# Performance work log

Measured on AMD Instinct MI355X. Metric: run time of the kernel, lower is better.

Reference implementation:

```python
import jax, jax.numpy as jnp
import numpy as np

D_MODEL = 1024
NUM_HEADS = 16
HEAD_DIM = D_MODEL // NUM_HEADS


def setup_inputs() -> dict:
    key = jax.random.key(0)
    ks = jax.random.split(key, 5)
    x = jax.random.normal(ks[0], (2, 2048, D_MODEL), dtype=jnp.float32)
    # torch nn.Linear init scale ~ U(-1/sqrt(in), 1/sqrt(in)); use small normals
    s = 1.0 / np.sqrt(D_MODEL)
    W_qkv = jax.random.normal(ks[1], (D_MODEL, 3 * D_MODEL), dtype=jnp.float32) * s
    b_qkv = jax.random.normal(ks[2], (3 * D_MODEL,), dtype=jnp.float32) * s
    W_out = jax.random.normal(ks[3], (D_MODEL, D_MODEL), dtype=jnp.float32) * s
    b_out = jax.random.normal(ks[4], (D_MODEL,), dtype=jnp.float32) * s
    return {"x": x, "W_qkv": W_qkv, "b_qkv": b_qkv, "W_out": W_out, "b_out": b_out}


def reference(x, W_qkv, b_qkv, W_out, b_out):
    B, S, _ = x.shape
    qkv = x @ W_qkv + b_qkv                                  # [B,S,3D]
    qkv = qkv.reshape(B, S, NUM_HEADS, 3 * HEAD_DIM).transpose(0, 2, 1, 3)  # [B,H,S,3d]
    q, k, v = jnp.split(qkv, 3, axis=-1)                     # each [B,H,S,d]
    scale = 1.0 / np.sqrt(HEAD_DIM)
    scores = jnp.einsum("bhqd,bhkd->bhqk", q, k) * scale      # [B,H,S,S]
    attn = jax.nn.softmax(scores, axis=-1)
    values = jnp.einsum("bhqk,bhkd->bhqd", attn, v)           # [B,H,S,d]
    values = values.transpose(0, 2, 1, 3).reshape(B, S, D_MODEL)
    return values @ W_out + b_out
```

## Files before the change

### kernel.cpp

```cpp
#include <hip/hip_runtime.h>


#define D_MODEL 1024
#define NHEAD   16
#define HDIM    64
#define SEQ     2048
#define BATCH   2
#define NTOK    (BATCH * SEQ)

typedef float    f32x4 __attribute__((ext_vector_type(4)));
typedef _Float16 f16x8 __attribute__((ext_vector_type(8)));
typedef _Float16 f16x4 __attribute__((ext_vector_type(4)));

#define GLOBAL_LOAD_LDS16(gptr, lptr)                                            \
    __builtin_amdgcn_global_load_lds(                                            \
        (const __attribute__((address_space(1))) unsigned int*)(gptr),           \
        (__attribute__((address_space(3))) unsigned int*)(lptr), 16, 0, 0)

__global__ __launch_bounds__(256) void prep_kernel(
    const float* __restrict__ x, _Float16* __restrict__ xh,
    const float* __restrict__ Wqkv, _Float16* __restrict__ wq_t,
    const float* __restrict__ Wout, _Float16* __restrict__ wo_t)
{
    const int bx = blockIdx.x;
    const int tid = threadIdx.x;
    if (bx < 4096) {
        const int i = (bx * 256 + tid) * 4;
        const float4 v = *(const float4*)&x[i];
        f16x4 hh;
        hh[0] = (_Float16)v.x; hh[1] = (_Float16)v.y;
        hh[2] = (_Float16)v.z; hh[3] = (_Float16)v.w;
        *(f16x4*)&xh[i] = hh;
        return;
    }
    __shared__ float ts[64][65];
    const float* W; _Float16* Wt; int N, n0, k0;
    if (bx < 4096 + 768) {
        const int local = bx - 4096;
        W = Wqkv; Wt = wq_t; N = 3072;
        n0 = (local % 48) * 64; k0 = (local / 48) * 64;
    } else {
        const int local = bx - 4864;
        W = Wout; Wt = wo_t; N = 1024;
        n0 = (local % 16) * 64; k0 = (local / 16) * 64;
    }
    {
        const int r = tid >> 2, c = (tid & 3) << 4;
        const float* src = W + (size_t)(k0 + r) * N + n0 + c;
        #pragma unroll
        for (int u = 0; u < 4; ++u)
            *(float4*)&ts[r][c + u * 4] = *(const float4*)&src[u * 4];
    }
    __syncthreads();
    {
        const int n = tid >> 2, kg = (tid & 3) << 4;
        f16x8 v0, v1;
        #pragma unroll
        for (int j = 0; j < 8; ++j) {
            v0[j] = (_Float16)ts[kg + j][n];
            v1[j] = (_Float16)ts[kg + 8 + j][n];
        }
        _Float16* dst = Wt + (size_t)(n0 + n) * D_MODEL + k0 + kg;
        *(f16x8*)&dst[0] = v0;
        *(f16x8*)&dst[8] = v1;
    }
}

__global__ __launch_bounds__(512) void gemm_qkv_kernel(
    const _Float16* __restrict__ A, const _Float16* __restrict__ Bt,
    const float* __restrict__ bias, _Float16* __restrict__ Cout,
    int M, int N, int K)
{
    __shared__ _Float16 lds[2][4096];
    const int tid = threadIdx.x;
    const int wave = tid >> 6, lane = tid & 63;
    const int quad = lane >> 4, l16 = lane & 15;
    const int m0 = blockIdx.y * 128, n0 = blockIdx.x * 128;
    const int wr = wave >> 1, wc = wave & 1;

    f32x4 acc[2][4] = {};

    const bool isA = wave < 4;
    const _Float16* gsrc = isA ? (A + (size_t)m0 * K) : (Bt + (size_t)n0 * K);
    _Float16* ldst = isA ? &lds[0][0] : &lds[1][0];
    const int sbase = (wave & 3) * 2;

    for (int k0 = 0; k0 < K; k0 += 32) {
        __syncthreads();
        #pragma unroll
        for (int j = 0; j < 2; ++j) {
            const int seg = sbase + j;
            const int chunk = seg >> 1;
            const int row = ((seg & 1) << 6) | lane;
            GLOBAL_LOAD_LDS16(gsrc + (size_t)row * K + k0 + chunk * 8, ldst + seg * 512);
        }
        __syncthreads();

        f16x8 a[2], b[4];
        #pragma unroll
        for (int mt = 0; mt < 2; ++mt)
            a[mt] = *(const f16x8*)&lds[0][quad * 1024 + (wr * 32 + mt * 16 + l16) * 8];
        #pragma unroll
        for (int nt = 0; nt < 4; ++nt)
            b[nt] = *(const f16x8*)&lds[1][quad * 1024 + (wc * 64 + nt * 16 + l16) * 8];
        #pragma unroll
        for (int mt = 0; mt < 2; ++mt)
            #pragma unroll
            for (int nt = 0; nt < 4; ++nt)
                acc[mt][nt] = __builtin_amdgcn_mfma_f32_16x16x32_f16(a[mt], b[nt], acc[mt][nt], 0, 0, 0);
    }

    #pragma unroll
    for (int nt = 0; nt < 4; ++nt) {
        const int col = n0 + wc * 64 + nt * 16 + l16;
        const float bv = bias[col];
        #pragma unroll
        for (int mt = 0; mt < 2; ++mt) {
            #pragma unroll
            for (int r = 0; r < 4; ++r) {
                const int row = m0 + wr * 32 + mt * 16 + quad * 4 + r;
                Cout[(size_t)row * N + col] = (_Float16)(acc[mt][nt][r] + bv);
            }
        }
    }
}

__global__ __launch_bounds__(512) void gemm_out_kernel(
    const _Float16* __restrict__ A, const _Float16* __restrict__ Bt,
    const float* __restrict__ bias, float* __restrict__ Cout)
{
    const int K = D_MODEL, N = D_MODEL;
    __shared__ _Float16 ldsA[4096];
    __shared__ _Float16 ldsB[2048];
    const int tid = threadIdx.x;
    const int wave = tid >> 6, lane = tid & 63;
    const int quad = lane >> 4, l16 = lane & 15;
    const int m0 = blockIdx.y * 128, n0 = blockIdx.x * 64;
    const int wr = wave >> 1, wc = wave & 1;

    f32x4 acc[2][2] = {};

    for (int k0 = 0; k0 < K; k0 += 32) {
        __syncthreads();
        if (wave < 4) {
            #pragma unroll
            for (int j = 0; j < 2; ++j) {
                const int seg = wave * 2 + j;
                const int chunk = seg >> 1;
                const int row = ((seg & 1) << 6) | lane;
                GLOBAL_LOAD_LDS16(A + (size_t)(m0 + row) * K + k0 + chunk * 8, ldsA + seg * 512);
            }
        } else {
            const int seg = wave - 4;
            GLOBAL_LOAD_LDS16(Bt + (size_t)(n0 + lane) * K + k0 + seg * 8, ldsB + seg * 512);
        }
        __syncthreads();

        f16x8 a[2], b[2];
        #pragma unroll
        for (int mt = 0; mt < 2; ++mt)
            a[mt] = *(const f16x8*)&ldsA[quad * 1024 + (wr * 32 + mt * 16 + l16) * 8];
        #pragma unroll
        for (int nt = 0; nt < 2; ++nt)
            b[nt] = *(const f16x8*)&ldsB[quad * 512 + (wc * 32 + nt * 16 + l16) * 8];
        #pragma unroll
        for (int mt = 0; mt < 2; ++mt)
            #pragma unroll
            for (int nt = 0; nt < 2; ++nt)
                acc[mt][nt] = __builtin_amdgcn_mfma_f32_16x16x32_f16(a[mt], b[nt], acc[mt][nt], 0, 0, 0);
    }

    #pragma unroll
    for (int nt = 0; nt < 2; ++nt) {
        const int col = n0 + wc * 32 + nt * 16 + l16;
        const float bv = bias[col];
        #pragma unroll
        for (int mt = 0; mt < 2; ++mt) {
            #pragma unroll
            for (int r = 0; r < 4; ++r) {
                const int row = m0 + wr * 32 + mt * 16 + quad * 4 + r;
                Cout[(size_t)row * N + col] = acc[mt][nt][r] + bv;
            }
        }
    }
}

__global__ __launch_bounds__(256) void swizzle_kv_kernel(
    const _Float16* __restrict__ qkv,
    _Float16* __restrict__ Ksw, _Float16* __restrict__ Vsw)
{
    __shared__ _Float16 ts[64][72];
    const int tid = threadIdx.x;
    const int s0 = blockIdx.x * 64, h = blockIdx.y, b = blockIdx.z;
    const size_t hsz = (size_t)8 * SEQ * 8;
    _Float16* kh = Ksw + (size_t)(b * NHEAD + h) * hsz;
    _Float16* vh = Vsw + (size_t)(b * NHEAD + h) * hsz;

    {
        const int s = s0 + (tid >> 2);
        const int dg = (tid & 3) << 4;
        const _Float16* src = qkv + (size_t)(b * SEQ + s) * (3 * D_MODEL) + h * (3 * HDIM) + HDIM + dg;
        const f16x8 v0 = *(const f16x8*)&src[0];
        const f16x8 v1 = *(const f16x8*)&src[8];
        const int c0 = dg >> 3;
        *(f16x8*)&kh[((size_t)c0 * SEQ + s) * 8]       = v0;
        *(f16x8*)&kh[((size_t)(c0 + 1) * SEQ + s) * 8] = v1;
    }
    {
        const int s = tid >> 2, dg = (tid & 3) << 4;
        const _Float16* src = qkv + (size_t)(b * SEQ + s0 + s) * (3 * D_MODEL) + h * (3 * HDIM) + 2 * HDIM + dg;
        *(f16x8*)&ts[s][dg]     = *(const f16x8*)&src[0];
        *(f16x8*)&ts[s][dg + 8] = *(const f16x8*)&src[8];
    }
    __syncthreads();
    {
        const int d = tid >> 2, sg = (tid & 3) << 4;
        f16x8 v0, v1;
        #pragma unroll
        for (int j = 0; j < 8; ++j) { v0[j] = ts[sg + j][d]; v1[j] = ts[sg + 8 + j][d]; }
        const int cs0 = (s0 + sg) >> 3;
        *(f16x8*)&vh[((size_t)cs0 * HDIM + d) * 8]       = v0;
        *(f16x8*)&vh[((size_t)(cs0 + 1) * HDIM + d) * 8] = v1;
    }
}

__global__ __launch_bounds__(256) void attn_mfma_kernel(
    const _Float16* __restrict__ qkv,
    const _Float16* __restrict__ Ksw, const _Float16* __restrict__ Vsw,
    _Float16* __restrict__ val)
{
    __shared__ _Float16 Ks[8 * 64 * 8];
    __shared__ _Float16 Vts[8 * 64 * 8];
    __shared__ _Float16 Ps[64 * 72];

    const int tid = threadIdx.x;
    const int wave = tid >> 6, lane = tid & 63;
    const int quad = lane >> 4, l16 = lane & 15;
    const int qt = blockIdx.x, h = blockIdx.y, b = blockIdx.z;
    const int q0 = qt * 64;

    const size_t hsz = (size_t)8 * SEQ * 8;
    const _Float16* kh = Ksw + (size_t)(b * NHEAD + h) * hsz;
    const _Float16* vh = Vsw + (size_t)(b * NHEAD + h) * hsz;

    f16x8 qf[2];
    {
        const int row = q0 + wave * 16 + l16;
        const _Float16* src = qkv + (size_t)(b * SEQ + row) * (3 * D_MODEL) + h * (3 * HDIM) + quad * 8;
        const f16x8 t0 = *(const f16x8*)(src);
        const f16x8 t1 = *(const f16x8*)(src + 32);
        #pragma unroll
        for (int j = 0; j < 8; ++j) {
            qf[0][j] = (_Float16)((float)t0[j] * 0.1803368802f);
            qf[1][j] = (_Float16)((float)t1[j] * 0.1803368802f);
        }
    }

    f32x4 acc[4] = {};
    float rs = 0.f;

    for (int kt = 0; kt < SEQ / 64; ++kt) {
        __syncthreads();
        #pragma unroll
        for (int jj = 0; jj < 2; ++jj) {
            const int c = wave * 2 + jj;
            GLOBAL_LOAD_LDS16(kh + ((size_t)c * SEQ + kt * 64 + lane) * 8, Ks + c * 512);
            GLOBAL_LOAD_LDS16(vh + ((size_t)(kt * 8 + c) * HDIM + lane) * 8, Vts + c * 512);
        }
        __syncthreads();

        f32x4 s[4] = {};
        #pragma unroll
        for (int mt = 0; mt < 4; ++mt) {
            const f16x8 kA0 = *(const f16x8*)&Ks[quad * 512 + (mt * 16 + l16) * 8];
            const f16x8 kA1 = *(const f16x8*)&Ks[(4 + quad) * 512 + (mt * 16 + l16) * 8];
            s[mt] = __builtin_amdgcn_mfma_f32_16x16x32_f16(kA0, qf[0], s[mt], 0, 0, 0);
            s[mt] = __builtin_amdgcn_mfma_f32_16x16x32_f16(kA1, qf[1], s[mt], 0, 0, 0);
        }

        #pragma unroll
        for (int mt = 0; mt < 4; ++mt) {
            const float p0 = __builtin_amdgcn_exp2f(s[mt][0]);
            const float p1 = __builtin_amdgcn_exp2f(s[mt][1]);
            const float p2 = __builtin_amdgcn_exp2f(s[mt][2]);
            const float p3 = __builtin_amdgcn_exp2f(s[mt][3]);
            rs += (p0 + p1) + (p2 + p3);
            uint2 w;
            w.x = __builtin_bit_cast(unsigned, __builtin_amdgcn_cvt_pkrtz(p0, p1));
            w.y = __builtin_bit_cast(unsigned, __builtin_amdgcn_cvt_pkrtz(p2, p3));
            *(uint2*)&Ps[(wave * 16 + l16) * 72 + mt * 16 + quad * 4] = w;
        }

        const f16x8 pA0 = *(const f16x8*)&Ps[(wave * 16 + l16) * 72 + quad * 8];
        const f16x8 pA1 = *(const f16x8*)&Ps[(wave * 16 + l16) * 72 + 32 + quad * 8];
        #pragma unroll
        for (int nt = 0; nt < 4; ++nt) {
            const f16x8 v0 = *(const f16x8*)&Vts[quad * 512 + (nt * 16 + l16) * 8];
            const f16x8 v1 = *(const f16x8*)&Vts[(4 + quad) * 512 + (nt * 16 + l16) * 8];
            acc[nt] = __builtin_amdgcn_mfma_f32_16x16x32_f16(pA0, v0, acc[nt], 0, 0, 0);
            acc[nt] = __builtin_amdgcn_mfma_f32_16x16x32_f16(pA1, v1, acc[nt], 0, 0, 0);
        }
    }

    rs += __shfl_xor(rs, 16);
    rs += __shfl_xor(rs, 32);
    const float inv = 1.f / rs;
    float invr[4];
    #pragma unroll
    for (int r = 0; r < 4; ++r)
        invr[r] = __shfl(inv, quad * 4 + r, 16);

    #pragma unroll
    for (int r = 0; r < 4; ++r) {
        const int row = b * SEQ + q0 + wave * 16 + quad * 4 + r;
        #pragma unroll
        for (int nt = 0; nt < 4; ++nt) {
            const int col = h * HDIM + nt * 16 + l16;
            val[(size_t)row * D_MODEL + col] = (_Float16)(acc[nt][r] * invr[r]);
        }
    }
}

extern "C" void kernel_launch(void* const* d_in, const int* in_sizes, int n_in,
                              void* d_out, int out_size, void* d_ws, size_t ws_size,
                              hipStream_t stream)
{
    const float* x     = (const float*)d_in[0];
    const float* W_qkv = (const float*)d_in[1];
    const float* b_qkv = (const float*)d_in[2];
    const float* W_out = (const float*)d_in[3];
    const float* b_out = (const float*)d_in[4];

    char* ws = (char*)d_ws;
    _Float16* Ksw   = (_Float16*)ws;
    _Float16* val_h = (_Float16*)(ws + (8u << 20));
    _Float16* wq_t  = (_Float16*)(ws + (16u << 20));
    _Float16* wo_t  = (_Float16*)(ws + (22u << 20));
    _Float16* qkv_h = (_Float16*)(ws + (24u << 20));
    _Float16* x_h   = (_Float16*)(ws + (48u << 20));
    _Float16* Vsw   = (_Float16*)(ws + (48u << 20));

    prep_kernel<<<5120, 256, 0, stream>>>(x, x_h, W_qkv, wq_t, W_out, wo_t);
    gemm_qkv_kernel<<<dim3(3 * D_MODEL / 128, NTOK / 128), 512, 0, stream>>>(
        x_h, wq_t, b_qkv, qkv_h, NTOK, 3 * D_MODEL, D_MODEL);
    swizzle_kv_kernel<<<dim3(SEQ / 64, NHEAD, BATCH), 256, 0, stream>>>(qkv_h, Ksw, Vsw);
    attn_mfma_kernel<<<dim3(SEQ / 64, NHEAD, BATCH), 256, 0, stream>>>(qkv_h, Ksw, Vsw, val_h);
    gemm_out_kernel<<<dim3(D_MODEL / 64, NTOK / 128), 512, 0, stream>>>(
        val_h, wo_t, b_out, (float*)d_out);
}
```

Baseline: 226.8 us.

## Split KV across waves in attention with cross-wave reduction and MFMA row sums

```diff
diff --git a/kernel.cpp b/kernel.cpp
--- a/kernel.cpp
+++ b/kernel.cpp
@@ -229,94 +229,141 @@
     const _Float16* __restrict__ Ksw, const _Float16* __restrict__ Vsw,
     _Float16* __restrict__ val)
 {
-    __shared__ _Float16 Ks[8 * 64 * 8];
-    __shared__ _Float16 Vts[8 * 64 * 8];
-    __shared__ _Float16 Ps[64 * 72];
+    __shared__ _Float16 Kst[8 * 128 * 8];
+    __shared__ _Float16 Vst[16 * 64 * 8];
+    __shared__ _Float16 Ps[4 * 64 * 40];
 
     const int tid = threadIdx.x;
     const int wave = tid >> 6, lane = tid & 63;
     const int quad = lane >> 4, l16 = lane & 15;
     const int qt = blockIdx.x, h = blockIdx.y, b = blockIdx.z;
     const int q0 = qt * 64;
+    const int wbase = wave * 32;
 
     const size_t hsz = (size_t)8 * SEQ * 8;
     const _Float16* kh = Ksw + (size_t)(b * NHEAD + h) * hsz;
     const _Float16* vh = Vsw + (size_t)(b * NHEAD + h) * hsz;
 
-    f16x8 qf[2];
-    {
-        const int row = q0 + wave * 16 + l16;
+    f16x8 qf[4][2];
+    #pragma unroll
+    for (int nt = 0; nt < 4; ++nt) {
+        const int row = q0 + nt * 16 + l16;
         const _Float16* src = qkv + (size_t)(b * SEQ + row) * (3 * D_MODEL) + h * (3 * HDIM) + quad * 8;
         const f16x8 t0 = *(const f16x8*)(src);
         const f16x8 t1 = *(const f16x8*)(src + 32);
         #pragma unroll
         for (int j = 0; j < 8; ++j) {
-            qf[0][j] = (_Float16)((float)t0[j] * 0.1803368802f);
-            qf[1][j] = (_Float16)((float)t1[j] * 0.1803368802f);
-        }
-    }
-
-    f32x4 acc[4] = {};
-    float rs = 0.f;
-
-    for (int kt = 0; kt < SEQ / 64; ++kt) {
-        __syncthreads();
-        #pragma unroll
-        for (int jj = 0; jj < 2; ++jj) {
-            const int c = wave * 2 + jj;
-            GLOBAL_LOAD_LDS16(kh + ((size_t)c * SEQ + kt * 64 + lane) * 8, Ks + c * 512);
-            GLOBAL_LOAD_LDS16(vh + ((size_t)(kt * 8 + c) * HDIM + lane) * 8, Vts + c * 512);
-        }
-        __syncthreads();
-
-        f32x4 s[4] = {};
-        #pragma unroll
-        for (int mt = 0; mt < 4; ++mt) {
-            const f16x8 kA0 = *(const f16x8*)&Ks[quad * 512 + (mt * 16 + l16) * 8];
-            const f16x8 kA1 = *(const f16x8*)&Ks[(4 + quad) * 512 + (mt * 16 + l16) * 8];
-            s[mt] = __builtin_amdgcn_mfma_f32_16x16x32_f16(kA0, qf[0], s[mt], 0, 0, 0);
-            s[mt] = __builtin_amdgcn_mfma_f32_16x16x32_f16(kA1, qf[1], s[mt], 0, 0, 0);
-        }
-
-        #pragma unroll
-        for (int mt = 0; mt < 4; ++mt) {
-            const float p0 = __builtin_amdgcn_exp2f(s[mt][0]);
-            const float p1 = __builtin_amdgcn_exp2f(s[mt][1]);
-            const float p2 = __builtin_amdgcn_exp2f(s[mt][2]);
-            const float p3 = __builtin_amdgcn_exp2f(s[mt][3]);
-            rs += (p0 + p1) + (p2 + p3);
-            uint2 w;
-            w.x = __builtin_bit_cast(unsigned, __builtin_amdgcn_cvt_pkrtz(p0, p1));
-            w.y = __builtin_bit_cast(unsigned, __builtin_amdgcn_cvt_pkrtz(p2, p3));
-            *(uint2*)&Ps[(wave * 16 + l16) * 72 + mt * 16 + quad * 4] = w;
-        }
-
-        const f16x8 pA0 = *(const f16x8*)&Ps[(wave * 16 + l16) * 72 + quad * 8];
-        const f16x8 pA1 = *(const f16x8*)&Ps[(wave * 16 + l16) * 72 + 32 + quad * 8];
-        #pragma unroll
-        for (int nt = 0; nt < 4; ++nt) {
-            const f16x8 v0 = *(const f16x8*)&Vts[quad * 512 + (nt * 16 + l16) * 8];
-            const f16x8 v1 = *(const f16x8*)&Vts[(4 + quad) * 512 + (nt * 16 + l16) * 8];
-            acc[nt] = __builtin_amdgcn_mfma_f32_16x16x32_f16(pA0, v0, acc[nt], 0, 0, 0);
-            acc[nt] = __builtin_amdgcn_mfma_f32_16x16x32_f16(pA1, v1, acc[nt], 0, 0, 0);
-        }
-    }
-
-    rs += __shfl_xor(rs, 16);
-    rs += __shfl_xor(rs, 32);
-    const float inv = 1.f / rs;
-    float invr[4];
+            qf[nt][0][j] = (_Float16)((float)t0[j] * 0.1803368802f);
+            qf[nt][1][j] = (_Float16)((float)t1[j] * 0.1803368802f);
+        }
+    }
+
+    f16x8 ones;
     #pragma unroll
-    for (int r = 0; r < 4; ++r)
-        invr[r] = __shfl(inv, quad * 4 + r, 16);
-
-    #pragma unroll
-    for (int r = 0; r < 4; ++r) {
-        const int row = b * SEQ + q0 + wave * 16 + quad * 4 + r;
-        #pragma unroll
-        for (int nt = 0; nt < 4; ++nt) {
-            const int col = h * HDIM + nt * 16 + l16;
-            val[(size_t)row * D_MODEL + col] = (_Float16)(acc[nt][r] * invr[r]);
+    for (int j = 0; j < 8; ++j) ones[j] = (_Float16)1.0f;
+
+    f32x4 acc[4][4] = {};
+    f32x4 lones[4] = {};
+
+    _Float16* psw = Ps + wave * (64 * 40);
+
+    for (int kt = 0; kt < SEQ / 128; ++kt) {
+        __syncthreads();
+        #pragma unroll
+        for (int j = 0; j < 4; ++j) {
+            const int kseg = wave * 4 + j;
+            const int c = kseg >> 1, half = kseg & 1;
+            GLOBAL_LOAD_LDS16(kh + ((size_t)c * SEQ + kt * 128 + half * 64 + lane) * 8,
+                              Kst + ((c * 128) + half * 64 + lane) * 8);
+            const int vs = wave * 4 + j;
+            GLOBAL_LOAD_LDS16(vh + ((size_t)(kt * 16 + vs) * 64 + lane) * 8,
+                              Vst + (vs * 64 + lane) * 8);
+        }
+        __syncthreads();
+
+        #pragma unroll
+        for (int mt = 0; mt < 2; ++mt) {
+            const int krow = wbase + mt * 16 + l16;
+            const f16x8 kA0 = *(const f16x8*)&Kst[((quad * 128) + krow) * 8];
+            const f16x8 kA1 = *(const f16x8*)&Kst[(((4 + quad) * 128) + krow) * 8];
+            f32x4 s[4] = {};
+            #pragma unroll
+            for (int nt = 0; nt < 4; ++nt) {
+                s[nt] = __builtin_amdgcn_mfma_f32_16x16x32_f16(kA0, qf[nt][0], s[nt], 0, 0, 0);
+                s[nt] = __builtin_amdgcn_mfma_f32_16x16x32_f16(kA1, qf[nt][1], s[nt], 0, 0, 0);
+            }
+            #pragma unroll
+            for (int nt = 0; nt < 4; ++nt) {
+                const float p0 = __builtin_amdgcn_exp2f(s[nt][0]);
+                const float p1 = __builtin_amdgcn_exp2f(s[nt][1]);
+                const float p2 = __builtin_amdgcn_exp2f(s[nt][2]);
+                const float p3 = __builtin_amdgcn_exp2f(s[nt][3]);
+                uint2 w;
+                w.x = __builtin_bit_cast(unsigned, __builtin_amdgcn_cvt_pkrtz(p0, p1));
+                w.y = __builtin_bit_cast(unsigned, __builtin_amdgcn_cvt_pkrtz(p2, p3));
+                *(uint2*)&psw[(nt * 16 + l16) * 40 + mt * 16 + quad * 4] = w;
+            }
+        }
+
+        f16x8 vf[4];
+        #pragma unroll
+        for (int nt = 0; nt < 4; ++nt)
+            vf[nt] = *(const f16x8*)&Vst[(((wave * 4 + quad) * 64) + nt * 16 + l16) * 8];
+        #pragma unroll
+        for (int mtile = 0; mtile < 4; ++mtile) {
+            const f16x8 pA = *(const f16x8*)&psw[(mtile * 16 + l16) * 40 + quad * 8];
+            #pragma unroll
+            for (int nt = 0; nt < 4; ++nt)
+                acc[mtile][nt] = __builtin_amdgcn_mfma_f32_16x16x32_f16(pA, vf[nt], acc[mtile][nt], 0, 0, 0);
+            lones[mtile] = __builtin_amdgcn_mfma_f32_16x16x32_f16(pA, ones, lones[mtile], 0, 0, 0);
+        }
+    }
+
+    __syncthreads();
+    float* sO = (float*)((wave & 1) ? Vst : Kst);
+    float* sL = ((float*)Ps) + ((wave & 1) ? 64 : 0);
+    if (wave < 2) {
+        #pragma unroll
+        for (int mtile = 0; mtile < 4; ++mtile) {
+            #pragma unroll
+            for (int r = 0; r < 4; ++r) {
+                const int row = mtile * 16 + quad * 4 + r;
+                #pragma unroll
+                for (int nt = 0; nt < 4; ++nt)
+                    sO[row * 64 + nt * 16 + l16] = acc[mtile][nt][r];
+                sL[row] = lones[mtile][r];
+            }
+        }
+    }
+    __syncthreads();
+    if (wave >= 2) {
+        #pragma unroll
+        for (int mtile = 0; mtile < 4; ++mtile) {
+            #pragma unroll
+            for (int r = 0; r < 4; ++r) {
+                const int row = mtile * 16 + quad * 4 + r;
+                #pragma unroll
+                for (int nt = 0; nt < 4; ++nt)
+                    sO[row * 64 + nt * 16 + l16] += acc[mtile][nt][r];
+                sL[row] += lones[mtile][r];
+            }
+        }
+    }
+    __syncthreads();
+    {
+        float* A0 = (float*)Kst; float* A1 = (float*)Vst;
+        float* L = (float*)Ps;
+        #pragma unroll
+        for (int r = 0; r < 4; ++r) {
+            const int row = wave * 16 + quad * 4 + r;
+            const float lt = L[row] + L[64 + row];
+            const float inv = 1.f / lt;
+            _Float16* dst = val + (size_t)(b * SEQ + q0 + row) * D_MODEL + h * HDIM;
+            #pragma unroll
+            for (int c = 0; c < 4; ++c) {
+                const int col = c * 16 + l16;
+                dst[col] = (_Float16)((A0[row * 64 + col] + A1[row * 64 + col]) * inv);
+            }
         }
     }
 }
```

New measurement: 249.0 us. +9.8%, slower.

## Split attention key tiles across waves and reduce partial outputs in LDS

Applied to the files above, without the earlier changes.

```diff
diff --git a/kernel.cpp b/kernel.cpp
--- a/kernel.cpp
+++ b/kernel.cpp
@@ -224,14 +224,15 @@
     }
 }
 
-__global__ __launch_bounds__(256) void attn_mfma_kernel(
+__global__ __launch_bounds__(256, 4) void attn_mfma_kernel(
     const _Float16* __restrict__ qkv,
     const _Float16* __restrict__ Ksw, const _Float16* __restrict__ Vsw,
     _Float16* __restrict__ val)
 {
-    __shared__ _Float16 Ks[8 * 64 * 8];
-    __shared__ _Float16 Vts[8 * 64 * 8];
-    __shared__ _Float16 Ps[64 * 72];
+    __shared__ _Float16 smem[13312];
+    _Float16* Kst = smem;
+    _Float16* Vst = smem + 4096;
+    _Float16* Ps  = smem + 8192;
 
     const int tid = threadIdx.x;
     const int wave = tid >> 6, lane = tid & 63;
@@ -243,81 +244,112 @@
     const _Float16* kh = Ksw + (size_t)(b * NHEAD + h) * hsz;
     const _Float16* vh = Vsw + (size_t)(b * NHEAD + h) * hsz;
 
-    f16x8 qf[2];
-    {
-        const int row = q0 + wave * 16 + l16;
+    f16x8 qf[4][2];
+    #pragma unroll
+    for (int nt = 0; nt < 4; ++nt) {
+        const int row = q0 + nt * 16 + l16;
         const _Float16* src = qkv + (size_t)(b * SEQ + row) * (3 * D_MODEL) + h * (3 * HDIM) + quad * 8;
         const f16x8 t0 = *(const f16x8*)(src);
         const f16x8 t1 = *(const f16x8*)(src + 32);
         #pragma unroll
         for (int j = 0; j < 8; ++j) {
-            qf[0][j] = (_Float16)((float)t0[j] * 0.1803368802f);
-            qf[1][j] = (_Float16)((float)t1[j] * 0.1803368802f);
-        }
-    }
-
-    f32x4 acc[4] = {};
-    float rs = 0.f;
+            qf[nt][0][j] = (_Float16)((float)t0[j] * 0.1803368802f);
+            qf[nt][1][j] = (_Float16)((float)t1[j] * 0.1803368802f);
+        }
+    }
+
+    f32x4 acc[4][4] = {};
+    float rs[4] = {};
+
+    _Float16* psw = Ps + wave * (64 * 20);
 
     for (int kt = 0; kt < SEQ / 64; ++kt) {
         __syncthreads();
         #pragma unroll
-        for (int jj = 0; jj < 2; ++jj) {
-            const int c = wave * 2 + jj;
-            GLOBAL_LOAD_LDS16(kh + ((size_t)c * SEQ + kt * 64 + lane) * 8, Ks + c * 512);
-            GLOBAL_LOAD_LDS16(vh + ((size_t)(kt * 8 + c) * HDIM + lane) * 8, Vts + c * 512);
-        }
-        __syncthreads();
-
-        f32x4 s[4] = {};
-        #pragma unroll
-        for (int mt = 0; mt < 4; ++mt) {
-            const f16x8 kA0 = *(const f16x8*)&Ks[quad * 512 + (mt * 16 + l16) * 8];
-            const f16x8 kA1 = *(const f16x8*)&Ks[(4 + quad) * 512 + (mt * 16 + l16) * 8];
-            s[mt] = __builtin_amdgcn_mfma_f32_16x16x32_f16(kA0, qf[0], s[mt], 0, 0, 0);
-            s[mt] = __builtin_amdgcn_mfma_f32_16x16x32_f16(kA1, qf[1], s[mt], 0, 0, 0);
-        }
-
-        #pragma unroll
-        for (int mt = 0; mt < 4; ++mt) {
-            const float p0 = __builtin_amdgcn_exp2f(s[mt][0]);
-            const float p1 = __builtin_amdgcn_exp2f(s[mt][1]);
-            const float p2 = __builtin_amdgcn_exp2f(s[mt][2]);
-            const float p3 = __builtin_amdgcn_exp2f(s[mt][3]);
-            rs += (p0 + p1) + (p2 + p3);
+        for (int j = 0; j < 2; ++j) {
+            const int c = wave * 2 + j;
+            GLOBAL_LOAD_LDS16(kh + ((size_t)c * SEQ + kt * 64 + lane) * 8, Kst + (c * 64 + lane) * 8);
+            GLOBAL_LOAD_LDS16(vh + ((size_t)(kt * 8 + c) * 64 + lane) * 8, Vst + (c * 64 + lane) * 8);
+        }
+        __syncthreads();
+
+        const f16x8 kA0 = *(const f16x8*)&Kst[(quad * 64 + wave * 16 + l16) * 8];
+        const f16x8 kA1 = *(const f16x8*)&Kst[((4 + quad) * 64 + wave * 16 + l16) * 8];
+        #pragma unroll
+        for (int nt = 0; nt < 4; ++nt) {
+            f32x4 s = {};
+            s = __builtin_amdgcn_mfma_f32_16x16x32_f16(kA0, qf[nt][0], s, 0, 0, 0);
+            s = __builtin_amdgcn_mfma_f32_16x16x32_f16(kA1, qf[nt][1], s, 0, 0, 0);
+            const float p0 = __builtin_amdgcn_exp2f(s[0]);
+            const float p1 = __builtin_amdgcn_exp2f(s[1]);
+            const float p2 = __builtin_amdgcn_exp2f(s[2]);
+            const float p3 = __builtin_amdgcn_exp2f(s[3]);
+            rs[nt] += (p0 + p1) + (p2 + p3);
             uint2 w;
             w.x = __builtin_bit_cast(unsigned, __builtin_amdgcn_cvt_pkrtz(p0, p1));
             w.y = __builtin_bit_cast(unsigned, __builtin_amdgcn_cvt_pkrtz(p2, p3));
-            *(uint2*)&Ps[(wave * 16 + l16) * 72 + mt * 16 + quad * 4] = w;
-        }
-
-        const f16x8 pA0 = *(const f16x8*)&Ps[(wave * 16 + l16) * 72 + quad * 8];
-        const f16x8 pA1 = *(const f16x8*)&Ps[(wave * 16 + l16) * 72 + 32 + quad * 8];
-        #pragma unroll
-        for (int nt = 0; nt < 4; ++nt) {
-            const f16x8 v0 = *(const f16x8*)&Vts[quad * 512 + (nt * 16 + l16) * 8];
-            const f16x8 v1 = *(const f16x8*)&Vts[(4 + quad) * 512 + (nt * 16 + l16) * 8];
-            acc[nt] = __builtin_amdgcn_mfma_f32_16x16x32_f16(pA0, v0, acc[nt], 0, 0, 0);
-            acc[nt] = __builtin_amdgcn_mfma_f32_16x16x32_f16(pA1, v1, acc[nt], 0, 0, 0);
-        }
-    }
-
-    rs += __shfl_xor(rs, 16);
-    rs += __shfl_xor(rs, 32);
-    const float inv = 1.f / rs;
-    float invr[4];
-    #pragma unroll
-    for (int r = 0; r < 4; ++r)
-        invr[r] = __shfl(inv, quad * 4 + r, 16);
-
-    #pragma unroll
-    for (int r = 0; r < 4; ++r) {
-        const int row = b * SEQ + q0 + wave * 16 + quad * 4 + r;
-        #pragma unroll
-        for (int nt = 0; nt < 4; ++nt) {
-            const int col = h * HDIM + nt * 16 + l16;
-            val[(size_t)row * D_MODEL + col] = (_Float16)(acc[nt][r] * invr[r]);
-        }
+            *(uint2*)&psw[(nt * 16 + l16) * 20 + quad * 4] = w;
+        }
+
+        f16x4 vf[4];
+        #pragma unroll
+        for (int nt = 0; nt < 4; ++nt)
+            vf[nt] = *(const f16x4*)&Vst[((wave * 2 + (quad >> 1)) * 64 + nt * 16 + l16) * 8 + (quad & 1) * 4];
+        #pragma unroll
+        for (int mtile = 0; mtile < 4; ++mtile) {
+            const f16x4 pA = *(const f16x4*)&psw[(mtile * 16 + l16) * 20 + quad * 4];
+            #pragma unroll
+            for (int nt = 0; nt < 4; ++nt)
+                acc[mtile][nt] = __builtin_amdgcn_mfma_f32_16x16x16f16(pA, vf[nt], acc[mtile][nt], 0, 0, 0);
+        }
+    }
+
+    __syncthreads();
+    float* sO = (float*)smem;
+    float* sL = (float*)(smem + 8192);
+
+    #pragma unroll
+    for (int nt = 0; nt < 4; ++nt) {
+        rs[nt] += __shfl_xor(rs[nt], 16);
+        rs[nt] += __shfl_xor(rs[nt], 32);
+    }
+    if (quad == 0) {
+        #pragma unroll
+        for (int nt = 0; nt < 4; ++nt)
+            sL[wave * 64 + nt * 16 + l16] = rs[nt];
+    }
+    #pragma unroll
+    for (int w = 0; w < 4; ++w) {
+        if (wave == w) {
+            #pragma unroll
+            for (int mtile = 0; mtile < 4; ++mtile)
+                #pragma unroll
+                for (int r = 0; r < 4; ++r) {
+                    const int row = mtile * 16 + quad * 4 + r;
+                    #pragma unroll
+                    for (int nt = 0; nt < 4; ++nt) {
+                        const int idx = row * 64 + nt * 16 + l16;
+                        if (w == 0) sO[idx] = acc[mtile][nt][r];
+                        else        sO[idx] += acc[mtile][nt][r];
+                    }
+                }
+        }
+        __syncthreads();
+    }
+
+    {
+        const int row = tid >> 2, cg = tid & 3;
+        const float l = sL[row] + sL[64 + row] + sL[128 + row] + sL[192 + row];
+        const float inv = 1.f / l;
+        f16x8 o0, o1;
+        #pragma unroll
+        for (int j = 0; j < 8; ++j) {
+            o0[j] = (_Float16)(sO[row * 64 + cg * 16 + j] * inv);
+            o1[j] = (_Float16)(sO[row * 64 + cg * 16 + 8 + j] * inv);
+        }
+        _Float16* dst = val + (size_t)(b * SEQ + q0 + row) * D_MODEL + h * HDIM + cg * 16;
+        *(f16x8*)&dst[0] = o0;
+        *(f16x8*)&dst[8] = o1;
     }
 }
 
```

Measured after the change: 256.1 us. 12.9% more time.
